# Performance work log

Measured on AMD Instinct MI355X. Metric: run time of the kernel, lower is better.

The kernel has to match this reference:

```python
import jax, jax.numpy as jnp
import numpy as np

B, T, I, H, L = 128, 1024, 256, 256, 2
P = 0.25  # dropout rate


def setup_inputs() -> dict:
    key = jax.random.key(0)
    ks = jax.random.split(key, 6)
    s = 1.0 / np.sqrt(H)  # PyTorch LSTMCell init range
    x = jax.random.normal(ks[0], (B, T, I), jnp.float32)
    W_ih = jax.random.uniform(ks[1], (L, 4 * H, I), jnp.float32, -s, s)
    W_hh = jax.random.uniform(ks[2], (L, 4 * H, H), jnp.float32, -s, s)
    b_ih = jax.random.uniform(ks[3], (L, 4 * H), jnp.float32, -s, s)
    b_hh = jax.random.uniform(ks[4], (L, 4 * H), jnp.float32, -s, s)
    # variational dropout masks: [L, 3, B, H] = (out, h, c) per layer, fixed over time
    keep = 1.0 - P
    masks = jax.random.bernoulli(ks[5], keep, (L, 3, B, H)).astype(jnp.float32) / keep
    return {"x": x, "W_ih": W_ih, "W_hh": W_hh, "b_ih": b_ih, "b_hh": b_hh, "masks": masks}


def _lstm_layer(x_tbi, W_ih, W_hh, b_ih, b_hh, out_m, h_m, c_m):
    # precompute input projection for all timesteps: [T, B, 4H]
    xp = jnp.einsum('tbi,gi->tbg', x_tbi, W_ih) + b_ih + b_hh
    h0 = jnp.zeros((x_tbi.shape[1], H), x_tbi.dtype)

    def step(carry, xp_t):
        h, c = carry
        gates = xp_t + h @ W_hh.T  # [B, 4H]
        i, f, g, o = jnp.split(gates, 4, axis=-1)  # PyTorch gate order i,f,g,o
        c2 = jax.nn.sigmoid(f) * c + jax.nn.sigmoid(i) * jnp.tanh(g)
        h2 = jax.nn.sigmoid(o) * jnp.tanh(c2)
        # variational dropout: output mask on emitted h, separate masks on carried h, c
        return (h2 * h_m, c2 * c_m), h2 * out_m

    _, y = jax.lax.scan(step, (h0, h0), xp)
    return y  # [T, B, H]


def reference(x, W_ih, W_hh, b_ih, b_hh, masks):
    y = jnp.transpose(x, (1, 0, 2))  # time-major [T, B, I]
    for l in range(L):
        y = _lstm_layer(y, W_ih[l], W_hh[l], b_ih[l], b_hh[l],
                        masks[l, 0], masks[l, 1], masks[l, 2])
    return jnp.transpose(y, (1, 0, 2))  # [B, T, H]
```

## Files before the change

### kernel.cpp

```cpp
#include <hip/hip_runtime.h>
#include <stdint.h>

#define BB 128
#define TT 1024
#define II 256
#define HH 256
#define G4 1024

#define Y1_DEPTH 16

typedef __attribute__((ext_vector_type(8))) short short8;
typedef __attribute__((ext_vector_type(4))) float float4v;

__device__ __forceinline__ unsigned short f2bf(float f) {
  union { float f; unsigned u; } v; v.f = f;
  unsigned u = v.u + 0x7FFFu + ((v.u >> 16) & 1u);
  return (unsigned short)(u >> 16);
}

__device__ __forceinline__ float sigm(float x) { return 1.f / (1.f + __expf(-x)); }
__device__ __forceinline__ float tanhfast(float x) { return 2.f / (1.f + __expf(-2.f * x)) - 1.f; }

__device__ __forceinline__ int poll_mall(const int* p) {
  int v;
  asm volatile("global_load_dword %0, %1, off sc0 sc1\n\ts_waitcnt vmcnt(0)"
               : "=v"(v) : "v"(p) : "memory");
  return v;
}
__device__ __forceinline__ short8 ld_mall_b128(const unsigned short* p) {
  short8 v;
  asm volatile("global_load_dwordx4 %0, %1, off sc0 sc1" : "=v"(v) : "v"(p));
  return v;
}
__device__ __forceinline__ void st_mall_u16(unsigned short* p, unsigned int v) {
  asm volatile("global_store_short %0, %1, off sc0 sc1" :: "v"(p), "v"(v) : "memory");
}
__device__ __forceinline__ void post_mall(int* p) {
  asm volatile("global_atomic_add %0, %1, off sc1" :: "v"(p), "v"(1) : "memory");
}

__global__ __launch_bounds__(256) void xprep(const float* __restrict__ x,
                                             unsigned short* __restrict__ xbf) {
  size_t i = ((size_t)blockIdx.x * 256 + threadIdx.x) * 8;
  int k = (int)(i & (size_t)(II - 1));
  size_t bt = i >> 8;
  int t = (int)(bt & (size_t)(TT - 1));
  int b = (int)(bt >> 10);
  float4v v0 = *(const float4v*)(x + i);
  float4v v1 = *(const float4v*)(x + i + 4);
  short8 s;
  s[0] = (short)f2bf(v0[0]); s[1] = (short)f2bf(v0[1]);
  s[2] = (short)f2bf(v0[2]); s[3] = (short)f2bf(v0[3]);
  s[4] = (short)f2bf(v1[0]); s[5] = (short)f2bf(v1[1]);
  s[6] = (short)f2bf(v1[2]); s[7] = (short)f2bf(v1[3]);
  *(short8*)(xbf + ((size_t)t * BB + b) * II + k) = s;
}

__global__ __launch_bounds__(256, 1) void vlstm(
    const float* __restrict__ x, const float* __restrict__ W_ih,
    const float* __restrict__ W_hh, const float* __restrict__ b_ih,
    const float* __restrict__ b_hh, const float* __restrict__ masks,
    float* __restrict__ out, int* __restrict__ flags,
    unsigned short* __restrict__ hstate, unsigned short* __restrict__ y1ring,
    const unsigned short* __restrict__ xbf, int use_xbf)
{
  const int tid = threadIdx.x;
  const int bid = blockIdx.x;
  const int layer = bid >> 5;
  const int bg = (bid >> 3) & 3;
  const int gs = bid & 7;
  const int bbase = bg * 32, jbase = gs * 32;

  __shared__ unsigned short Wlds[128][520];
  __shared__ float gsh[32][136];
  __shared__ float bias_sh[128];

  const float* Wih_l = W_ih + (size_t)layer * G4 * II;
  const float* Whh_l = W_hh + (size_t)layer * G4 * HH;
  for (int e = tid; e < 128 * 512; e += 256) {
    int n = e >> 9, c = e & 511;
    int r = (n & 3) * HH + jbase + (n >> 2);
    float w = (c < 256) ? Wih_l[(size_t)r * II + c] : Whh_l[(size_t)r * HH + (c - 256)];
    Wlds[n][c] = f2bf(w);
  }
  if (tid < 128) {
    int r = (tid & 3) * HH + jbase + (tid >> 2);
    bias_sh[tid] = b_ih[layer * G4 + r] + b_hh[layer * G4 + r];
  }

  float cst[4], m_out[4], m_h[4], m_c[4];
  const float* mk = masks + (size_t)layer * 3 * BB * HH;
  #pragma unroll
  for (int r = 0; r < 4; ++r) {
    int idx = r * 256 + tid;
    int m = idx >> 5, jl = idx & 31;
    int b = bbase + m, j = jbase + jl;
    m_out[r] = mk[(size_t)b * HH + j];
    m_h[r]   = mk[(size_t)BB * HH + (size_t)b * HH + j];
    m_c[r]   = mk[(size_t)2 * BB * HH + (size_t)b * HH + j];
    cst[r] = 0.f;
  }
  __syncthreads();

  const int wv = tid >> 6;
  const int lane = tid & 63;
  const int lr = lane & 15;
  const int lg = lane >> 4;

  int* fown = flags + (layer * 4 + bg) * TT;
  int* fin  = flags + bg * TT;
  int* fl2  = flags + (4 + bg) * TT;
  unsigned short* hs_l = hstate + (size_t)layer * 2 * BB * HH;

  int budget = 1 << 23;

  #pragma unroll 1
  for (int t = 0; t < TT; ++t) {
    short8 afrag[2][16];
    if (layer == 0) {
      #pragma unroll
      for (int mt = 0; mt < 2; ++mt) {
        const int b = bbase + mt * 16 + lr;
        if (use_xbf) {
          const unsigned short* xp = xbf + ((size_t)t * BB + b) * II + lg * 8;
          #pragma unroll
          for (int kt = 0; kt < 8; ++kt)
            afrag[mt][kt] = *(const short8*)(xp + kt * 32);
        } else {
          const float* xp = x + ((size_t)b * TT + t) * II + lg * 8;
          #pragma unroll
          for (int kt = 0; kt < 8; ++kt) {
            float4v v0 = *(const float4v*)(xp + kt * 32);
            float4v v1 = *(const float4v*)(xp + kt * 32 + 4);
            short8 s;
            s[0] = (short)f2bf(v0[0]); s[1] = (short)f2bf(v0[1]);
            s[2] = (short)f2bf(v0[2]); s[3] = (short)f2bf(v0[3]);
            s[4] = (short)f2bf(v1[0]); s[5] = (short)f2bf(v1[1]);
            s[6] = (short)f2bf(v1[2]); s[7] = (short)f2bf(v1[3]);
            afrag[mt][kt] = s;
          }
        }
      }
    }

    if (tid == 0) {
      if (t > 0)           while (budget > 0) { --budget; if (poll_mall(fown + t - 1) >= 8) break; }
      if (layer == 1)      { while (budget > 0) { --budget; if (poll_mall(fin + t) >= 8) break; } }
      else if (t >= Y1_DEPTH) { while (budget > 0) { --budget; if (poll_mall(fl2 + t - Y1_DEPTH) >= 8) break; } }
    }
    __syncthreads();

    const unsigned short* hread = hs_l + (size_t)((t + 1) & 1) * BB * HH;

    #pragma unroll
    for (int mt = 0; mt < 2; ++mt) {
      const int b = bbase + mt * 16 + lr;
      if (layer == 1) {
        const unsigned short* yp =
            y1ring + ((size_t)(t & (Y1_DEPTH - 1)) * BB + b) * HH + lg * 8;
        #pragma unroll
        for (int kt = 0; kt < 8; ++kt) afrag[mt][kt] = ld_mall_b128(yp + kt * 32);
      }
      const unsigned short* hp = hread + (size_t)b * HH + lg * 8;
      #pragma unroll
      for (int kt = 0; kt < 8; ++kt) afrag[mt][8 + kt] = ld_mall_b128(hp + kt * 32);
    }
    asm volatile("s_waitcnt vmcnt(0)" ::: "memory");
    __builtin_amdgcn_sched_barrier(0);

    float4v acc[2][2] = {};
    #pragma unroll
    for (int kt = 0; kt < 16; ++kt) {
      #pragma unroll
      for (int nt = 0; nt < 2; ++nt) {
        short8 bfrag = *(const short8*)&Wlds[wv * 32 + nt * 16 + lr][kt * 32 + lg * 8];
        #pragma unroll
        for (int mt = 0; mt < 2; ++mt)
          acc[mt][nt] = __builtin_amdgcn_mfma_f32_16x16x32_bf16(
              afrag[mt][kt], bfrag, acc[mt][nt], 0, 0, 0);
      }
    }

    #pragma unroll
    for (int mt = 0; mt < 2; ++mt)
      #pragma unroll
      for (int nt = 0; nt < 2; ++nt)
        #pragma unroll
        for (int rg = 0; rg < 4; ++rg)
          gsh[mt * 16 + lg * 4 + rg][wv * 32 + nt * 16 + lr] = acc[mt][nt][rg];
    __syncthreads();

    unsigned short* hwrite = hs_l + (size_t)(t & 1) * BB * HH;
    #pragma unroll
    for (int r = 0; r < 4; ++r) {
      int idx = r * 256 + tid;
      int m = idx >> 5, jl = idx & 31;
      float4v g4 = *(const float4v*)&gsh[m][jl * 4];
      float gi = sigm(g4[0] + bias_sh[jl * 4 + 0]);
      float gf = sigm(g4[1] + bias_sh[jl * 4 + 1]);
      float gg = tanhfast(g4[2] + bias_sh[jl * 4 + 2]);
      float go = sigm(g4[3] + bias_sh[jl * 4 + 3]);
      float c2 = gf * cst[r] + gi * gg;
      float h2 = go * tanhfast(c2);
      cst[r] = c2 * m_c[r];
      int b = bbase + m, j = jbase + jl;
      st_mall_u16(&hwrite[(size_t)b * HH + j], f2bf(h2 * m_h[r]));
      if (layer == 0)
        st_mall_u16(&y1ring[((size_t)(t & (Y1_DEPTH - 1)) * BB + b) * HH + j],
                    f2bf(h2 * m_out[r]));
      else
        out[((size_t)b * TT + t) * HH + j] = h2 * m_out[r];
    }
    asm volatile("s_waitcnt vmcnt(0)" ::: "memory");
    __syncthreads();
    if (tid == 0) post_mall(fown + t);
  }
}

extern "C" void kernel_launch(void* const* d_in, const int* in_sizes, int n_in,
                              void* d_out, int out_size, void* d_ws, size_t ws_size,
                              hipStream_t stream) {
  const float* x     = (const float*)d_in[0];
  const float* W_ih  = (const float*)d_in[1];
  const float* W_hh  = (const float*)d_in[2];
  const float* b_ih  = (const float*)d_in[3];
  const float* b_hh  = (const float*)d_in[4];
  const float* masks = (const float*)d_in[5];
  float* out = (float*)d_out;

  const size_t FLAG_BYTES = (size_t)2 * 4 * TT * sizeof(int);
  const size_t HS_BYTES   = (size_t)2 * 2 * BB * HH * sizeof(unsigned short);
  const size_t Y1_BYTES   = (size_t)Y1_DEPTH * BB * HH * sizeof(unsigned short);
  const size_t BASE       = FLAG_BYTES + HS_BYTES + Y1_BYTES;
  const size_t XBF_BYTES  = (size_t)TT * BB * II * sizeof(unsigned short);
  const int use_xbf = (ws_size >= BASE + XBF_BYTES) ? 1 : 0;

  int* flags = (int*)d_ws;
  unsigned short* hstate = (unsigned short*)((char*)d_ws + FLAG_BYTES);
  unsigned short* y1ring = (unsigned short*)((char*)d_ws + FLAG_BYTES + HS_BYTES);
  unsigned short* xbf    = (unsigned short*)((char*)d_ws + BASE);

  hipMemsetAsync(d_ws, 0, BASE, stream);
  if (use_xbf)
    xprep<<<dim3((BB * TT * II / 8) / 256), dim3(256), 0, stream>>>(x, xbf);
  vlstm<<<dim3(64), dim3(256), 0, stream>>>(x, W_ih, W_hh, b_ih, b_hh, masks,
                                            out, flags, hstate, y1ring,
                                            xbf, use_xbf);
}
```

Before: 7.482 ms.

## Restructure LSTM step sync with batched flag polling, prefetch and packed stores

Each thread now handles four contiguous hidden units, so the h, y1 and output writes become packed 64-bit bf16 or 128-bit float stores instead of scattered 16-bit stores. Flag waiting issues all needed flag loads together, double-buffered, in place of serial polls. Separate cross-layer flags let layer 1 prefetch y1 for the next step before the barrier when it is already ready. Layer 0 prefetches the next step's x fragments after posting its flag. The end-of-step barrier waits with vmcnt(1), leaving one store outstanding, which adds memory-ordering risk to the per-step handoff chain in exchange for less latency on the sequential critical path.

```diff
diff --git a/kernel.cpp b/kernel.cpp
--- a/kernel.cpp
+++ b/kernel.cpp
@@ -17,23 +17,21 @@
   unsigned u = v.u + 0x7FFFu + ((v.u >> 16) & 1u);
   return (unsigned short)(u >> 16);
 }
-
 __device__ __forceinline__ float sigm(float x) { return 1.f / (1.f + __expf(-x)); }
 __device__ __forceinline__ float tanhfast(float x) { return 2.f / (1.f + __expf(-2.f * x)) - 1.f; }
 
-__device__ __forceinline__ int poll_mall(const int* p) {
-  int v;
-  asm volatile("global_load_dword %0, %1, off sc0 sc1\n\ts_waitcnt vmcnt(0)"
-               : "=v"(v) : "v"(p) : "memory");
-  return v;
-}
-__device__ __forceinline__ short8 ld_mall_b128(const unsigned short* p) {
+__device__ __forceinline__ unsigned long long pack4bf(float a, float b, float c, float d) {
+  return (unsigned long long)f2bf(a) | ((unsigned long long)f2bf(b) << 16) |
+         ((unsigned long long)f2bf(c) << 32) | ((unsigned long long)f2bf(d) << 48);
+}
+
+__device__ __forceinline__ short8 ld128_mall(const unsigned short* p) {
   short8 v;
   asm volatile("global_load_dwordx4 %0, %1, off sc0 sc1" : "=v"(v) : "v"(p));
   return v;
 }
-__device__ __forceinline__ void st_mall_u16(unsigned short* p, unsigned int v) {
-  asm volatile("global_store_short %0, %1, off sc0 sc1" :: "v"(p), "v"(v) : "memory");
+__device__ __forceinline__ void st64_mall(unsigned short* p, unsigned long long v) {
+  asm volatile("global_store_dwordx2 %0, %1, off sc0 sc1" :: "v"(p), "v"(v) : "memory");
 }
 __device__ __forceinline__ void post_mall(int* p) {
   asm volatile("global_atomic_add %0, %1, off sc1" :: "v"(p), "v"(1) : "memory");
@@ -72,8 +70,11 @@
   const int bbase = bg * 32, jbase = gs * 32;
 
   __shared__ unsigned short Wlds[128][520];
-  __shared__ float gsh[32][136];
+  __shared__ float gsh[32][132];
   __shared__ float bias_sh[128];
+  __shared__ int s_y1n[2];
+
+  if (tid == 0) { s_y1n[0] = 0; s_y1n[1] = 0; }
 
   const float* Wih_l = W_ih + (size_t)layer * G4 * II;
   const float* Whh_l = W_hh + (size_t)layer * G4 * HH;
@@ -88,65 +89,123 @@
     bias_sh[tid] = b_ih[layer * G4 + r] + b_hh[layer * G4 + r];
   }
 
-  float cst[4], m_out[4], m_h[4], m_c[4];
-  const float* mk = masks + (size_t)layer * 3 * BB * HH;
-  #pragma unroll
-  for (int r = 0; r < 4; ++r) {
-    int idx = r * 256 + tid;
-    int m = idx >> 5, jl = idx & 31;
-    int b = bbase + m, j = jbase + jl;
-    m_out[r] = mk[(size_t)b * HH + j];
-    m_h[r]   = mk[(size_t)BB * HH + (size_t)b * HH + j];
-    m_c[r]   = mk[(size_t)2 * BB * HH + (size_t)b * HH + j];
-    cst[r] = 0.f;
-  }
-  __syncthreads();
-
   const int wv = tid >> 6;
   const int lane = tid & 63;
   const int lr = lane & 15;
   const int lg = lane >> 4;
+  const int em = tid >> 3;
+  const int eq = tid & 7;
+
+  float cst[4], m_out[4], m_h[4], m_c[4];
+  {
+    const float* mk = masks + (size_t)layer * 3 * BB * HH;
+    #pragma unroll
+    for (int r = 0; r < 4; ++r) {
+      int b = bbase + em, j = jbase + eq * 4 + r;
+      m_out[r] = mk[(size_t)b * HH + j];
+      m_h[r]   = mk[(size_t)BB * HH + (size_t)b * HH + j];
+      m_c[r]   = mk[(size_t)2 * BB * HH + (size_t)b * HH + j];
+      cst[r] = 0.f;
+    }
+  }
+  __syncthreads();
 
   int* fown = flags + (layer * 4 + bg) * TT;
-  int* fin  = flags + bg * TT;
-  int* fl2  = flags + (4 + bg) * TT;
+  int* fcA  = flags + (8 + bg) * TT;
+  int* fcB  = flags + (12 + bg) * TT;
   unsigned short* hs_l = hstate + (size_t)layer * 2 * BB * HH;
 
-  int budget = 1 << 23;
+  short8 afrag[2][16];
+  auto load_afx = [&](int t) {
+    #pragma unroll
+    for (int mt = 0; mt < 2; ++mt) {
+      const int b = bbase + mt * 16 + lr;
+      if (use_xbf) {
+        const unsigned short* xp = xbf + ((size_t)t * BB + b) * II + lg * 8;
+        #pragma unroll
+        for (int kt = 0; kt < 8; ++kt)
+          afrag[mt][kt] = *(const short8*)(xp + kt * 32);
+      } else {
+        const float* xp = x + ((size_t)b * TT + t) * II + lg * 8;
+        #pragma unroll
+        for (int kt = 0; kt < 8; ++kt) {
+          float4v v0 = *(const float4v*)(xp + kt * 32);
+          float4v v1 = *(const float4v*)(xp + kt * 32 + 4);
+          short8 s;
+          s[0] = (short)f2bf(v0[0]); s[1] = (short)f2bf(v0[1]);
+          s[2] = (short)f2bf(v0[2]); s[3] = (short)f2bf(v0[3]);
+          s[4] = (short)f2bf(v1[0]); s[5] = (short)f2bf(v1[1]);
+          s[6] = (short)f2bf(v1[2]); s[7] = (short)f2bf(v1[3]);
+          afrag[mt][kt] = s;
+        }
+      }
+    }
+  };
+  if (layer == 0) load_afx(0);
+
+  int budget = 1 << 24;
 
   #pragma unroll 1
   for (int t = 0; t < TT; ++t) {
-    short8 afrag[2][16];
-    if (layer == 0) {
-      #pragma unroll
-      for (int mt = 0; mt < 2; ++mt) {
-        const int b = bbase + mt * 16 + lr;
-        if (use_xbf) {
-          const unsigned short* xp = xbf + ((size_t)t * BB + b) * II + lg * 8;
+    int y1pre = 0;
+    if (layer == 1) {
+      y1pre = s_y1n[t & 1];
+      if (y1pre) {
+        #pragma unroll
+        for (int mt = 0; mt < 2; ++mt) {
+          const unsigned short* yp =
+              y1ring + ((size_t)(t & (Y1_DEPTH - 1)) * BB + bbase + mt * 16 + lr) * HH + lg * 8;
           #pragma unroll
           for (int kt = 0; kt < 8; ++kt)
-            afrag[mt][kt] = *(const short8*)(xp + kt * 32);
-        } else {
-          const float* xp = x + ((size_t)b * TT + t) * II + lg * 8;
-          #pragma unroll
-          for (int kt = 0; kt < 8; ++kt) {
-            float4v v0 = *(const float4v*)(xp + kt * 32);
-            float4v v1 = *(const float4v*)(xp + kt * 32 + 4);
-            short8 s;
-            s[0] = (short)f2bf(v0[0]); s[1] = (short)f2bf(v0[1]);
-            s[2] = (short)f2bf(v0[2]); s[3] = (short)f2bf(v0[3]);
-            s[4] = (short)f2bf(v1[0]); s[5] = (short)f2bf(v1[1]);
-            s[6] = (short)f2bf(v1[2]); s[7] = (short)f2bf(v1[3]);
-            afrag[mt][kt] = s;
-          }
+            afrag[mt][kt] = ld128_mall(yp + kt * 32);
         }
       }
     }
 
     if (tid == 0) {
-      if (t > 0)           while (budget > 0) { --budget; if (poll_mall(fown + t - 1) >= 8) break; }
-      if (layer == 1)      { while (budget > 0) { --budget; if (poll_mall(fin + t) >= 8) break; } }
-      else if (t >= Y1_DEPTH) { while (budget > 0) { --budget; if (poll_mall(fl2 + t - Y1_DEPTH) >= 8) break; } }
+      int need_own = (t > 0) ? 1 : 0;
+      int need_in  = (layer == 1) ? 1 : 0;
+      int need_sl  = (layer == 0 && t >= Y1_DEPTH) ? 1 : 0;
+      const int probe = (layer == 1 && t + 1 < TT) ? 1 : 0;
+      int y1n = 0;
+      if (need_own | need_in | need_sl) {
+        const int* w0 = need_own ? fown + (t - 1)      : fown + t;
+        const int* w1 = need_in  ? fcA + t             : fown + t;
+        const int* w2 = need_sl  ? fcB + (t - Y1_DEPTH): fown + t;
+        const int* w3 = probe    ? fcA + (t + 1)       : fown + t;
+        int a0, a1, a2, a3, b0, b1, b2, b3;
+#define ISSUE4(r0, r1, r2, r3)                                   \
+        asm volatile("global_load_dword %0, %4, off sc0 sc1\n\t" \
+                     "global_load_dword %1, %5, off sc0 sc1\n\t" \
+                     "global_load_dword %2, %6, off sc0 sc1\n\t" \
+                     "global_load_dword %3, %7, off sc0 sc1"     \
+                     : "=&v"(r0), "=&v"(r1), "=&v"(r2), "=&v"(r3)\
+                     : "v"(w0), "v"(w1), "v"(w2), "v"(w3) : "memory")
+        ISSUE4(a0, a1, a2, a3);
+        ISSUE4(b0, b1, b2, b3);
+        while (true) {
+          asm volatile("s_waitcnt vmcnt(4)" ::: "memory");
+          __builtin_amdgcn_sched_barrier(0);
+          if (a0 >= 8) need_own = 0;
+          if (a1 >= 8) need_in  = 0;
+          if (a2 >= 8) need_sl  = 0;
+          if (a3 >= 8) y1n = 1;
+          if (!(need_own | need_in | need_sl)) break;
+          if (--budget < 0) break;
+          ISSUE4(a0, a1, a2, a3);
+          asm volatile("s_waitcnt vmcnt(4)" ::: "memory");
+          __builtin_amdgcn_sched_barrier(0);
+          if (b0 >= 8) need_own = 0;
+          if (b1 >= 8) need_in  = 0;
+          if (b2 >= 8) need_sl  = 0;
+          if (b3 >= 8) y1n = 1;
+          if (!(need_own | need_in | need_sl)) break;
+          if (--budget < 0) break;
+          ISSUE4(b0, b1, b2, b3);
+        }
+#undef ISSUE4
+      }
+      s_y1n[(t + 1) & 1] = y1n;
     }
     __syncthreads();
 
@@ -155,15 +214,16 @@
     #pragma unroll
     for (int mt = 0; mt < 2; ++mt) {
       const int b = bbase + mt * 16 + lr;
-      if (layer == 1) {
+      if (layer == 1 && !y1pre) {
         const unsigned short* yp =
             y1ring + ((size_t)(t & (Y1_DEPTH - 1)) * BB + b) * HH + lg * 8;
         #pragma unroll
-        for (int kt = 0; kt < 8; ++kt) afrag[mt][kt] = ld_mall_b128(yp + kt * 32);
+        for (int kt = 0; kt < 8; ++kt) afrag[mt][kt] = ld128_mall(yp + kt * 32);
       }
       const unsigned short* hp = hread + (size_t)b * HH + lg * 8;
       #pragma unroll
-      for (int kt = 0; kt < 8; ++kt) afrag[mt][8 + kt] = ld_mall_b128(hp + kt * 32);
+      for (int kt = 0; kt < 8; ++kt)
+        afrag[mt][8 + kt] = ld128_mall(hp + kt * 32);
     }
     asm volatile("s_waitcnt vmcnt(0)" ::: "memory");
     __builtin_amdgcn_sched_barrier(0);
@@ -188,33 +248,53 @@
         #pragma unroll
         for (int rg = 0; rg < 4; ++rg)
           gsh[mt * 16 + lg * 4 + rg][wv * 32 + nt * 16 + lr] = acc[mt][nt][rg];
-    __syncthreads();
+    asm volatile("s_waitcnt lgkmcnt(0)" ::: "memory");
+    __builtin_amdgcn_s_barrier();
+    __builtin_amdgcn_sched_barrier(0);
 
     unsigned short* hwrite = hs_l + (size_t)(t & 1) * BB * HH;
+    float hh2[4];
     #pragma unroll
     for (int r = 0; r < 4; ++r) {
-      int idx = r * 256 + tid;
-      int m = idx >> 5, jl = idx & 31;
-      float4v g4 = *(const float4v*)&gsh[m][jl * 4];
-      float gi = sigm(g4[0] + bias_sh[jl * 4 + 0]);
-      float gf = sigm(g4[1] + bias_sh[jl * 4 + 1]);
-      float gg = tanhfast(g4[2] + bias_sh[jl * 4 + 2]);
-      float go = sigm(g4[3] + bias_sh[jl * 4 + 3]);
+      float4v g4 = *(const float4v*)&gsh[em][eq * 16 + r * 4];
+      float gi = sigm(g4[0] + bias_sh[eq * 16 + r * 4 + 0]);
+      float gf = sigm(g4[1] + bias_sh[eq * 16 + r * 4 + 1]);
+      float gg = tanhfast(g4[2] + bias_sh[eq * 16 + r * 4 + 2]);
+      float go = sigm(g4[3] + bias_sh[eq * 16 + r * 4 + 3]);
       float c2 = gf * cst[r] + gi * gg;
-      float h2 = go * tanhfast(c2);
+      hh2[r] = go * tanhfast(c2);
       cst[r] = c2 * m_c[r];
-      int b = bbase + m, j = jbase + jl;
-      st_mall_u16(&hwrite[(size_t)b * HH + j], f2bf(h2 * m_h[r]));
-      if (layer == 0)
-        st_mall_u16(&y1ring[((size_t)(t & (Y1_DEPTH - 1)) * BB + b) * HH + j],
-                    f2bf(h2 * m_out[r]));
-      else
-        out[((size_t)b * TT + t) * HH + j] = h2 * m_out[r];
-    }
-    asm volatile("s_waitcnt vmcnt(0)" ::: "memory");
-    __syncthreads();
-    if (tid == 0) post_mall(fown + t);
+    }
+    {
+      unsigned long long hp4 = pack4bf(hh2[0] * m_h[0], hh2[1] * m_h[1],
+                                       hh2[2] * m_h[2], hh2[3] * m_h[3]);
+      st64_mall(hwrite + (size_t)(bbase + em) * HH + jbase + eq * 4, hp4);
+      if (layer == 0) {
+        unsigned long long yp4 = pack4bf(hh2[0] * m_out[0], hh2[1] * m_out[1],
+                                         hh2[2] * m_out[2], hh2[3] * m_out[3]);
+        st64_mall(y1ring + ((size_t)(t & (Y1_DEPTH - 1)) * BB + bbase + em) * HH
+                      + jbase + eq * 4, yp4);
+      } else {
+        float4v ov;
+        ov[0] = hh2[0] * m_out[0]; ov[1] = hh2[1] * m_out[1];
+        ov[2] = hh2[2] * m_out[2]; ov[3] = hh2[3] * m_out[3];
+        *(float4v*)(out + ((size_t)(bbase + em) * TT + t) * HH + jbase + eq * 4) = ov;
+      }
+    }
+    asm volatile("s_waitcnt vmcnt(1) lgkmcnt(0)" ::: "memory");
+    __builtin_amdgcn_s_barrier();
+    __builtin_amdgcn_sched_barrier(0);
+    if (tid == 0) {
+      post_mall(fown + t);
+      if (layer == 0) { if (t > 0) post_mall(fcA + (t - 1)); }
+      else post_mall(fcB + t);
+    }
+    if (layer == 0 && t + 1 < TT) load_afx(t + 1);
   }
+
+  asm volatile("s_waitcnt vmcnt(0)" ::: "memory");
+  __syncthreads();
+  if (tid == 0 && layer == 0) post_mall(fcA + (TT - 1));
 }
 
 extern "C" void kernel_launch(void* const* d_in, const int* in_sizes, int n_in,
@@ -228,7 +308,7 @@
   const float* masks = (const float*)d_in[5];
   float* out = (float*)d_out;
 
-  const size_t FLAG_BYTES = (size_t)2 * 4 * TT * sizeof(int);
+  const size_t FLAG_BYTES = (size_t)16 * TT * sizeof(int);
   const size_t HS_BYTES   = (size_t)2 * 2 * BB * HH * sizeof(unsigned short);
   const size_t Y1_BYTES   = (size_t)Y1_DEPTH * BB * HH * sizeof(unsigned short);
   const size_t BASE       = FLAG_BYTES + HS_BYTES + Y1_BYTES;
```

After: 6.875 ms. 1.09x faster.
